# Kernel tuning notes

Measured on AMD Instinct MI355X. Metric: run time of the kernel, lower is better.

## Reference

```python
import jax, jax.numpy as jnp
import numpy as np

B, L, H, T = 128, 512, 512, 24
START, STOP = T - 2, T - 1
NEG = -10000.0


def setup_inputs() -> dict:
    key = jax.random.key(0)
    k1, k2, k3, k4 = jax.random.split(key, 4)
    features = jax.random.normal(k1, (B, L, H), dtype=jnp.float32)
    emission_w = jax.random.normal(k2, (T, H), dtype=jnp.float32) * 0.02
    emission_b = jnp.zeros((T,), dtype=jnp.float32)
    transitions = jax.random.normal(k3, (T, T), dtype=jnp.float32)
    # CRF constraints: nothing transitions INTO START; nothing transitions OUT of STOP
    # (transitions[i, j] = score of transitioning j -> i, per the forward_alg indexing)
    transitions = transitions.at[START, :].set(NEG).at[:, STOP].set(NEG)
    lengths = jax.random.randint(k4, (B,), 1, L + 1)
    return {"features": features, "emission_w": emission_w,
            "emission_b": emission_b, "transitions": transitions,
            "lengths": lengths}


def reference(features, emission_w, emission_b, transitions, lengths):
    # emission scores: [B, L, T]
    emit = jnp.einsum('blh,th->blt', features, emission_w) + emission_b
    Bn, Ln, Tn = emit.shape
    # init alphas: -10000 everywhere except START tag
    fv0 = jnp.full((Bn, Tn), NEG, dtype=emit.dtype).at[:, START].set(0.0)

    def step(fv, xs):
        e_t, t = xs  # e_t: [B, T], t: scalar timestep
        # tag_var[b, j, k] = emit[b, j] + transitions[j, k] + fv[b, k]
        scores = e_t[:, :, None] + transitions[None, :, :] + fv[:, None, :]
        new = jax.nn.logsumexp(scores, axis=2)  # [B, T]
        # only advance sequences that haven't ended (equivalent to gathering
        # forward_var at index lengths[b] in the original)
        fv = jnp.where((t < lengths)[:, None], new, fv)
        return fv, None

    fv, _ = jax.lax.scan(step, fv0, (jnp.swapaxes(emit, 0, 1), jnp.arange(Ln)))
    terminal = fv + transitions[STOP][None, :]
    return jax.nn.logsumexp(terminal, axis=1)  # alpha: [B]
```

## Files before the change

kernel.cpp:

```cpp
#include <hip/hip_runtime.h>
#include <hip/hip_bf16.h>

typedef unsigned int uint;
typedef unsigned short ushort;

#define Bn 128
#define Ln 512
#define Hn 512
#define Tn 24
#define START_TAG 22
#define STOP_TAG 23
#define NCH 16
#define CHL 32

using frag_ab = __attribute__((ext_vector_type(8))) short;
using frag_cd = __attribute__((ext_vector_type(4))) float;
union ABU { frag_ab f; uint u[4]; };

#define PACKW(x, y) \
  __builtin_amdgcn_perm(__float_as_uint(y), __float_as_uint(x), 0x07060302u)
#define MFMA16 __builtin_amdgcn_mfma_f32_16x16x32_bf16

__device__ __forceinline__ float bf2f(ushort v) {
  return __uint_as_float(((uint)v) << 16);
}
__device__ __forceinline__ float rlf(float v, int l) {
  return __int_as_float(__builtin_amdgcn_readlane(__float_as_int(v), l));
}
__device__ __forceinline__ float rfl(float v) {
  return __int_as_float(__builtin_amdgcn_readfirstlane(__float_as_int(v)));
}
__device__ __forceinline__ uint bperm(int addr, uint v) {
  return (uint)__builtin_amdgcn_ds_bpermute(addr, (int)v);
}

__global__ __launch_bounds__(128) void fused_kernel(
    const float* __restrict__ feat, const float* __restrict__ W,
    const float* __restrict__ bias, const float* __restrict__ trans,
    const int* __restrict__ lengths, ushort* __restrict__ G,
    float* __restrict__ Rc, float* __restrict__ u0buf) {
  __shared__ float ee[CHL][28];
  const int bid = blockIdx.x;
  const int b = bid >> 4, c = bid & 15;
  const int wv = threadIdx.x >> 6, l = threadIdx.x & 63;
  const int ct = l & 15, g = l >> 4;
  const int ct2 = 16 + (ct & 7);

  const float* fp = feat + (size_t)(bid * CHL + wv * 16 + ct) * Hn + 8 * g;
  const float* wp0 = W + ct * Hn + 8 * g;
  const float* wp1 = W + ct2 * Hn + 8 * g;
  frag_cd acc0 = {0.f, 0.f, 0.f, 0.f}, acc1 = {0.f, 0.f, 0.f, 0.f};
#pragma unroll 2
  for (int kk = 0; kk < 16; ++kk) {
    const int off = kk * 32;
    float4 fa = *(const float4*)(fp + off);
    float4 fb = *(const float4*)(fp + off + 4);
    float4 wa0 = *(const float4*)(wp0 + off);
    float4 wb0 = *(const float4*)(wp0 + off + 4);
    float4 wa1 = *(const float4*)(wp1 + off);
    float4 wb1 = *(const float4*)(wp1 + off + 4);
    ABU A, B0, B1;
    A.u[0] = PACKW(fa.x, fa.y);  A.u[1] = PACKW(fa.z, fa.w);
    A.u[2] = PACKW(fb.x, fb.y);  A.u[3] = PACKW(fb.z, fb.w);
    B0.u[0] = PACKW(wa0.x, wa0.y); B0.u[1] = PACKW(wa0.z, wa0.w);
    B0.u[2] = PACKW(wb0.x, wb0.y); B0.u[3] = PACKW(wb0.z, wb0.w);
    B1.u[0] = PACKW(wa1.x, wa1.y); B1.u[1] = PACKW(wa1.z, wa1.w);
    B1.u[2] = PACKW(wb1.x, wb1.y); B1.u[3] = PACKW(wb1.z, wb1.w);
    acc0 = MFMA16(A.f, B0.f, acc0, 0, 0, 0);
    acc1 = MFMA16(A.f, B1.f, acc1, 0, 0, 0);
  }
  const float bs0 = bias[ct];
  const float bs1 = bias[ct2];
  const int rr = wv * 16 + 4 * g;
#pragma unroll
  for (int r = 0; r < 4; ++r) {
    ee[rr + r][ct] = __expf(acc0[r] + bs0);
    if (ct < 8) ee[rr + r][16 + ct] = __expf(acc1[r] + bs1);
  }
  __syncthreads();
  if (c == 0 && threadIdx.x < Tn)
    u0buf[b * Tn + threadIdx.x] = ee[0][threadIdx.x];

  const int cw = (bid >> 8) & 1;
  if (wv != cw) return;

  const int len = lengths[b];
  const int lo = (c == 0) ? 1 : 0;
  int hi = len - c * CHL;
  if (hi > CHL) hi = CHL;

  float E0[8], E1[8];
#pragma unroll
  for (int i = 0; i < 8; ++i) {
    int k = 8 * g + i;
    int kc = k < 23 ? k : 23;
    E0[i] = (k < Tn) ? __expf(trans[ct * Tn + kc]) : 0.f;
    E1[i] = (k < Tn && ct < 8) ? __expf(trans[ct2 * Tn + kc]) : 0.f;
  }

  frag_cd D00, D01, D10, D11;
#pragma unroll
  for (int r = 0; r < 4; ++r) {
    float dv = (4 * g + r == ct) ? 1.f : 0.f;
    D00[r] = dv; D11[r] = dv; D01[r] = 0.f; D10[r] = 0.f;
  }

  float R = 0.f;
  const int addr0 = (ct + 32 * (g & 1)) * 4;
  const int addr1 = addr0 + 64;
  const bool mhi = (g >= 2);

#define RENORMF()                                                       \
  do {                                                                  \
    float ref = fmaxf(fmaxf(D00[0], D00[1]), fmaxf(D00[2], D00[3]));    \
    ref = rfl(ref);                                                     \
    int ebx = ((__float_as_int(ref) >> 23) & 255) - 127;                \
    float sc = __int_as_float((uint)(127 - ebx) << 23);                 \
    _Pragma("unroll") for (int r = 0; r < 4; ++r) {                     \
      D00[r] *= sc; D01[r] *= sc; D10[r] *= sc; D11[r] *= sc;           \
    }                                                                   \
    R += (float)ebx * 0.6931471805599453f;                              \
  } while (0)

  int stepc = 0;
  for (int lt = lo; lt < hi; ++lt) {
    float ea = ee[lt][ct];
    float eb = ee[lt][ct2];
    uint p000 = PACKW(D00[0], D00[1]), p001 = PACKW(D00[2], D00[3]);
    uint p010 = PACKW(D01[0], D01[1]), p011 = PACKW(D01[2], D01[3]);
    uint p100 = PACKW(D10[0], D10[1]), p101 = PACKW(D10[2], D10[3]);
    uint p110 = PACKW(D11[0], D11[1]), p111 = PACKW(D11[2], D11[3]);
    ABU Bf0, Bf1;
    {
      uint a0 = bperm(addr0, p000), b0 = bperm(addr0, p100);
      uint a1 = bperm(addr0, p001), b1 = bperm(addr0, p101);
      uint a2 = bperm(addr1, p000), b2 = bperm(addr1, p100);
      uint a3 = bperm(addr1, p001), b3 = bperm(addr1, p101);
      Bf0.u[0] = mhi ? b0 : a0;
      Bf0.u[1] = mhi ? b1 : a1;
      Bf0.u[2] = mhi ? b2 : a2;
      Bf0.u[3] = mhi ? b3 : a3;
      a0 = bperm(addr0, p010); b0 = bperm(addr0, p110);
      a1 = bperm(addr0, p011); b1 = bperm(addr0, p111);
      a2 = bperm(addr1, p010); b2 = bperm(addr1, p110);
      a3 = bperm(addr1, p011); b3 = bperm(addr1, p111);
      Bf1.u[0] = mhi ? b0 : a0;
      Bf1.u[1] = mhi ? b1 : a1;
      Bf1.u[2] = mhi ? b2 : a2;
      Bf1.u[3] = mhi ? b3 : a3;
    }
    ABU A0, A1;
    A0.u[0] = PACKW(ea * E0[0], ea * E0[1]);
    A0.u[1] = PACKW(ea * E0[2], ea * E0[3]);
    A0.u[2] = PACKW(ea * E0[4], ea * E0[5]);
    A0.u[3] = PACKW(ea * E0[6], ea * E0[7]);
    A1.u[0] = PACKW(eb * E1[0], eb * E1[1]);
    A1.u[1] = PACKW(eb * E1[2], eb * E1[3]);
    A1.u[2] = PACKW(eb * E1[4], eb * E1[5]);
    A1.u[3] = PACKW(eb * E1[6], eb * E1[7]);
    frag_cd z = {0.f, 0.f, 0.f, 0.f};
    D00 = MFMA16(A0.f, Bf0.f, z, 0, 0, 0);
    D01 = MFMA16(A0.f, Bf1.f, z, 0, 0, 0);
    D10 = MFMA16(A1.f, Bf0.f, z, 0, 0, 0);
    D11 = MFMA16(A1.f, Bf1.f, z, 0, 0, 0);
    if ((++stepc & 3) == 0) RENORMF();
  }
  RENORMF();

  ushort* Gc = G + (size_t)bid * 1024;
  uint2 w2;
  w2.x = PACKW(D00[0], D00[1]); w2.y = PACKW(D00[2], D00[3]);
  *(uint2*)(Gc + ct * 32 + 4 * g) = w2;
  w2.x = PACKW(D01[0], D01[1]); w2.y = PACKW(D01[2], D01[3]);
  *(uint2*)(Gc + (16 + ct) * 32 + 4 * g) = w2;
  w2.x = PACKW(D10[0], D10[1]); w2.y = PACKW(D10[2], D10[3]);
  *(uint2*)(Gc + ct * 32 + 16 + 4 * g) = w2;
  w2.x = PACKW(D11[0], D11[1]); w2.y = PACKW(D11[2], D11[3]);
  *(uint2*)(Gc + (16 + ct) * 32 + 16 + 4 * g) = w2;
  if (l == 0) Rc[bid] = R;
}

__global__ __launch_bounds__(64) void passB(
    const float* __restrict__ trans, const ushort* __restrict__ G,
    const float* __restrict__ Rc, const float* __restrict__ u0buf,
    float* __restrict__ out) {
  const int b = blockIdx.x;
  const int j = threadIdx.x;
  const bool act = j < Tn;
  const int jj = act ? j : 0;

  float v = act ? u0buf[b * Tn + jj] * __expf(trans[jj * Tn + START_TAG]) : 0.f;
  float R = 0.f;
  const ushort* Gb = G + (size_t)b * (NCH * 1024);

#pragma unroll 1
  for (int c = 0; c < NCH; ++c) {
    const ushort* Gc = Gb + c * 1024;
    float p[24];
#pragma unroll
    for (int k = 0; k < 24; ++k) p[k] = bf2f(Gc[k * 32 + jj]);
    float s = 0.f;
#pragma unroll
    for (int k = 0; k < 24; ++k) s = fmaf(p[k], rlf(v, k), s);
    v = act ? s : 0.f;
    R += Rc[b * NCH + c];
    float ref = rfl(v);
    int ebx = ((__float_as_int(ref) >> 23) & 255) - 127;
    v *= __int_as_float((uint)(127 - ebx) << 23);
    R += (float)ebx * 0.6931471805599453f;
  }

  float term = act ? v * __expf(trans[STOP_TAG * Tn + jj]) : 0.f;
  term += __shfl_xor(term, 1, 64);
  term += __shfl_xor(term, 2, 64);
  term += __shfl_xor(term, 4, 64);
  term += __shfl_xor(term, 8, 64);
  term += __shfl_xor(term, 16, 64);
  term += __shfl_xor(term, 32, 64);
  if (j == 0) out[b] = R + logf(term);
}

extern "C" void kernel_launch(void* const* d_in, const int* in_sizes, int n_in,
                              void* d_out, int out_size, void* d_ws,
                              size_t ws_size, hipStream_t stream) {
  const float* feat = (const float*)d_in[0];
  const float* W = (const float*)d_in[1];
  const float* bias = (const float*)d_in[2];
  const float* trans = (const float*)d_in[3];
  const int* lengths = (const int*)d_in[4];
  float* out = (float*)d_out;

  ushort* G = (ushort*)d_ws;
  float* Rc = (float*)((char*)d_ws + 4194304);
  float* u0buf = (float*)((char*)d_ws + 4202496);

  fused_kernel<<<Bn * NCH, 128, 0, stream>>>(feat, W, bias, trans, lengths, G,
                                             Rc, u0buf);
  passB<<<Bn, 64, 0, stream>>>(trans, G, Rc, u0buf, out);
}
```

Measured before the change: 224.8 us.

## Shorten scan chunks, give each wave its own chunk, pre-convert W to bf16

The sequence is now split into 32 chunks of 16 steps instead of 16 chunks of 32, and each of the four waves in a 256-thread block computes emissions for and scans its own chunk, so no wave sits idle after the GEMM. The emission weights are converted to bf16 once by a small new kernel, which removes per-iteration packing of W in the GEMM. The per-step A operand becomes the constant exp(transitions) matrix, with the emission scaling applied to the MFMA outputs from LDS afterwards. The costs are an extra kernel launch and a serial passB that now combines twice as many chunk matrices.

```diff
diff --git a/kernel.cpp b/kernel.cpp
--- a/kernel.cpp
+++ b/kernel.cpp
@@ -10,8 +10,8 @@
 #define Tn 24
 #define START_TAG 22
 #define STOP_TAG 23
-#define NCH 16
-#define CHL 32
+#define NCH 32
+#define CHL 16
 
 using frag_ab = __attribute__((ext_vector_type(8))) short;
 using frag_cd = __attribute__((ext_vector_type(4))) float;
@@ -24,6 +24,10 @@
 __device__ __forceinline__ float bf2f(ushort v) {
   return __uint_as_float(((uint)v) << 16);
 }
+__device__ __forceinline__ ushort f2bf_rne(float x) {
+  uint u = __float_as_uint(x);
+  return (ushort)((u + 0x7FFFu + ((u >> 16) & 1u)) >> 16);
+}
 __device__ __forceinline__ float rlf(float v, int l) {
   return __int_as_float(__builtin_amdgcn_readlane(__float_as_int(v), l));
 }
@@ -34,69 +38,70 @@
   return (uint)__builtin_amdgcn_ds_bpermute(addr, (int)v);
 }
 
-__global__ __launch_bounds__(128) void fused_kernel(
-    const float* __restrict__ feat, const float* __restrict__ W,
+__global__ __launch_bounds__(256) void wconv(const float* __restrict__ W,
+                                             ushort* __restrict__ Wbf) {
+  int i = blockIdx.x * 256 + threadIdx.x;
+  if (i < Tn * Hn) Wbf[i] = f2bf_rne(W[i]);
+}
+
+__global__ __launch_bounds__(256, 4) void fused_kernel(
+    const float* __restrict__ feat, const ushort* __restrict__ Wbf,
     const float* __restrict__ bias, const float* __restrict__ trans,
     const int* __restrict__ lengths, ushort* __restrict__ G,
     float* __restrict__ Rc, float* __restrict__ u0buf) {
-  __shared__ float ee[CHL][28];
-  const int bid = blockIdx.x;
-  const int b = bid >> 4, c = bid & 15;
+  __shared__ float ee[4][CHL][32];
   const int wv = threadIdx.x >> 6, l = threadIdx.x & 63;
   const int ct = l & 15, g = l >> 4;
-  const int ct2 = 16 + (ct & 7);
-
-  const float* fp = feat + (size_t)(bid * CHL + wv * 16 + ct) * Hn + 8 * g;
-  const float* wp0 = W + ct * Hn + 8 * g;
-  const float* wp1 = W + ct2 * Hn + 8 * g;
+  const int chunk = blockIdx.x * 4 + wv;
+  const int b = chunk >> 5, c = chunk & 31;
+
+  const float* fp = feat + (size_t)(chunk * CHL + ct) * Hn + 8 * g;
+  const ushort* wp0 = Wbf + ct * Hn + 8 * g;
+  const ushort* wp1 = Wbf + (16 + (ct & 7)) * Hn + 8 * g;
   frag_cd acc0 = {0.f, 0.f, 0.f, 0.f}, acc1 = {0.f, 0.f, 0.f, 0.f};
-#pragma unroll 2
+#pragma unroll 4
   for (int kk = 0; kk < 16; ++kk) {
-    const int off = kk * 32;
-    float4 fa = *(const float4*)(fp + off);
-    float4 fb = *(const float4*)(fp + off + 4);
-    float4 wa0 = *(const float4*)(wp0 + off);
-    float4 wb0 = *(const float4*)(wp0 + off + 4);
-    float4 wa1 = *(const float4*)(wp1 + off);
-    float4 wb1 = *(const float4*)(wp1 + off + 4);
-    ABU A, B0, B1;
-    A.u[0] = PACKW(fa.x, fa.y);  A.u[1] = PACKW(fa.z, fa.w);
-    A.u[2] = PACKW(fb.x, fb.y);  A.u[3] = PACKW(fb.z, fb.w);
-    B0.u[0] = PACKW(wa0.x, wa0.y); B0.u[1] = PACKW(wa0.z, wa0.w);
-    B0.u[2] = PACKW(wb0.x, wb0.y); B0.u[3] = PACKW(wb0.z, wb0.w);
-    B1.u[0] = PACKW(wa1.x, wa1.y); B1.u[1] = PACKW(wa1.z, wa1.w);
-    B1.u[2] = PACKW(wb1.x, wb1.y); B1.u[3] = PACKW(wb1.z, wb1.w);
-    acc0 = MFMA16(A.f, B0.f, acc0, 0, 0, 0);
-    acc1 = MFMA16(A.f, B1.f, acc1, 0, 0, 0);
+    float4 fa = *(const float4*)(fp + kk * 32);
+    float4 fb = *(const float4*)(fp + kk * 32 + 4);
+    frag_ab b0 = *(const frag_ab*)(wp0 + kk * 32);
+    frag_ab b1 = *(const frag_ab*)(wp1 + kk * 32);
+    ABU A;
+    A.u[0] = PACKW(fa.x, fa.y);
+    A.u[1] = PACKW(fa.z, fa.w);
+    A.u[2] = PACKW(fb.x, fb.y);
+    A.u[3] = PACKW(fb.z, fb.w);
+    acc0 = MFMA16(A.f, b0, acc0, 0, 0, 0);
+    acc1 = MFMA16(A.f, b1, acc1, 0, 0, 0);
   }
   const float bs0 = bias[ct];
-  const float bs1 = bias[ct2];
-  const int rr = wv * 16 + 4 * g;
+  const float bs1 = bias[16 + (ct & 7)];
 #pragma unroll
   for (int r = 0; r < 4; ++r) {
-    ee[rr + r][ct] = __expf(acc0[r] + bs0);
-    if (ct < 8) ee[rr + r][16 + ct] = __expf(acc1[r] + bs1);
+    ee[wv][4 * g + r][ct] = __expf(acc0[r] + bs0);
+    if (ct < 8) {
+      ee[wv][4 * g + r][16 + ct] = __expf(acc1[r] + bs1);
+      ee[wv][4 * g + r][24 + ct] = 0.f;
+    }
   }
   __syncthreads();
-  if (c == 0 && threadIdx.x < Tn)
-    u0buf[b * Tn + threadIdx.x] = ee[0][threadIdx.x];
-
-  const int cw = (bid >> 8) & 1;
-  if (wv != cw) return;
+  if (c == 0 && l < Tn) u0buf[b * Tn + l] = ee[wv][0][l];
+
+  ABU A0c, A1c;
+#pragma unroll
+  for (int h = 0; h < 4; ++h) {
+    int k0 = 8 * g + 2 * h, k1 = k0 + 1;
+    float e00 = (k0 < Tn) ? __expf(trans[ct * Tn + k0]) : 0.f;
+    float e01 = (k1 < Tn) ? __expf(trans[ct * Tn + k1]) : 0.f;
+    A0c.u[h] = PACKW(e00, e01);
+    float e10 = (k0 < Tn && ct < 8) ? __expf(trans[(16 + ct) * Tn + k0]) : 0.f;
+    float e11 = (k1 < Tn && ct < 8) ? __expf(trans[(16 + ct) * Tn + k1]) : 0.f;
+    A1c.u[h] = PACKW(e10, e11);
+  }
 
   const int len = lengths[b];
   const int lo = (c == 0) ? 1 : 0;
   int hi = len - c * CHL;
   if (hi > CHL) hi = CHL;
-
-  float E0[8], E1[8];
-#pragma unroll
-  for (int i = 0; i < 8; ++i) {
-    int k = 8 * g + i;
-    int kc = k < 23 ? k : 23;
-    E0[i] = (k < Tn) ? __expf(trans[ct * Tn + kc]) : 0.f;
-    E1[i] = (k < Tn && ct < 8) ? __expf(trans[ct2 * Tn + kc]) : 0.f;
-  }
 
   frag_cd D00, D01, D10, D11;
 #pragma unroll
@@ -124,8 +129,6 @@
 
   int stepc = 0;
   for (int lt = lo; lt < hi; ++lt) {
-    float ea = ee[lt][ct];
-    float eb = ee[lt][ct2];
     uint p000 = PACKW(D00[0], D00[1]), p001 = PACKW(D00[2], D00[3]);
     uint p010 = PACKW(D01[0], D01[1]), p011 = PACKW(D01[2], D01[3]);
     uint p100 = PACKW(D10[0], D10[1]), p101 = PACKW(D10[2], D10[3]);
@@ -149,25 +152,26 @@
       Bf1.u[2] = mhi ? b2 : a2;
       Bf1.u[3] = mhi ? b3 : a3;
     }
-    ABU A0, A1;
-    A0.u[0] = PACKW(ea * E0[0], ea * E0[1]);
-    A0.u[1] = PACKW(ea * E0[2], ea * E0[3]);
-    A0.u[2] = PACKW(ea * E0[4], ea * E0[5]);
-    A0.u[3] = PACKW(ea * E0[6], ea * E0[7]);
-    A1.u[0] = PACKW(eb * E1[0], eb * E1[1]);
-    A1.u[1] = PACKW(eb * E1[2], eb * E1[3]);
-    A1.u[2] = PACKW(eb * E1[4], eb * E1[5]);
-    A1.u[3] = PACKW(eb * E1[6], eb * E1[7]);
     frag_cd z = {0.f, 0.f, 0.f, 0.f};
-    D00 = MFMA16(A0.f, Bf0.f, z, 0, 0, 0);
-    D01 = MFMA16(A0.f, Bf1.f, z, 0, 0, 0);
-    D10 = MFMA16(A1.f, Bf0.f, z, 0, 0, 0);
-    D11 = MFMA16(A1.f, Bf1.f, z, 0, 0, 0);
+    frag_cd N00 = MFMA16(A0c.f, Bf0.f, z, 0, 0, 0);
+    frag_cd N01 = MFMA16(A0c.f, Bf1.f, z, 0, 0, 0);
+    frag_cd N10 = MFMA16(A1c.f, Bf0.f, z, 0, 0, 0);
+    frag_cd N11 = MFMA16(A1c.f, Bf1.f, z, 0, 0, 0);
+    float4 s0 = *(const float4*)(&ee[wv][lt][4 * g]);
+    float4 s1 = *(const float4*)(&ee[wv][lt][16 + 4 * g]);
+    D00[0] = N00[0] * s0.x; D00[1] = N00[1] * s0.y;
+    D00[2] = N00[2] * s0.z; D00[3] = N00[3] * s0.w;
+    D01[0] = N01[0] * s0.x; D01[1] = N01[1] * s0.y;
+    D01[2] = N01[2] * s0.z; D01[3] = N01[3] * s0.w;
+    D10[0] = N10[0] * s1.x; D10[1] = N10[1] * s1.y;
+    D10[2] = N10[2] * s1.z; D10[3] = N10[3] * s1.w;
+    D11[0] = N11[0] * s1.x; D11[1] = N11[1] * s1.y;
+    D11[2] = N11[2] * s1.z; D11[3] = N11[3] * s1.w;
     if ((++stepc & 3) == 0) RENORMF();
   }
   RENORMF();
 
-  ushort* Gc = G + (size_t)bid * 1024;
+  ushort* Gc = G + (size_t)chunk * 1024;
   uint2 w2;
   w2.x = PACKW(D00[0], D00[1]); w2.y = PACKW(D00[2], D00[3]);
   *(uint2*)(Gc + ct * 32 + 4 * g) = w2;
@@ -177,7 +181,7 @@
   *(uint2*)(Gc + ct * 32 + 16 + 4 * g) = w2;
   w2.x = PACKW(D11[0], D11[1]); w2.y = PACKW(D11[2], D11[3]);
   *(uint2*)(Gc + (16 + ct) * 32 + 16 + 4 * g) = w2;
-  if (l == 0) Rc[bid] = R;
+  if (l == 0) Rc[chunk] = R;
 }
 
 __global__ __launch_bounds__(64) void passB(
@@ -231,10 +235,12 @@
   float* out = (float*)d_out;
 
   ushort* G = (ushort*)d_ws;
-  float* Rc = (float*)((char*)d_ws + 4194304);
-  float* u0buf = (float*)((char*)d_ws + 4202496);
-
-  fused_kernel<<<Bn * NCH, 128, 0, stream>>>(feat, W, bias, trans, lengths, G,
-                                             Rc, u0buf);
+  float* Rc = (float*)((char*)d_ws + 8388608);
+  float* u0buf = (float*)((char*)d_ws + 8404992);
+  ushort* Wbf = (ushort*)((char*)d_ws + 8417280);
+
+  wconv<<<48, 256, 0, stream>>>(W, Wbf);
+  fused_kernel<<<Bn * NCH / 4, 256, 0, stream>>>(feat, Wbf, bias, trans,
+                                                 lengths, G, Rc, u0buf);
   passB<<<Bn, 64, 0, stream>>>(trans, G, Rc, u0buf, out);
 }
```

Measured after the change: 233.7 us. +4.0%, slower.
